# Kernel optimization log

Hardware: AMD Instinct MI355X
Metric: run time of the kernel (lower is better)

## Reference

```python
import jax, jax.numpy as jnp
import numpy as np

H = 51      # lstm_out, hard-coded in the module
L = 3       # num_lstms
IN = 2      # input_dim = f_in(1) + f_time(1)
B = 1024
T = 2048


def _softplus(x):
    # log(1+exp(x)) with the module's inf guard (softplus==inf -> x),
    # written in a grad-safe clipped form (identical in fp32 range).
    x_safe = jnp.minimum(x, 30.0)
    return jnp.where(x > 30.0, x, jnp.log1p(jnp.exp(x_safe)))


def setup_inputs() -> dict:
    key = jax.random.key(0)
    ks = jax.random.split(key, 2 + 4 * L + 2)
    inp = {}
    inp["input"] = jax.random.normal(ks[0], (B, T, 1), dtype=jnp.float32)
    inp["time_idx"] = jax.random.normal(ks[1], (B, T, 1), dtype=jnp.float32)
    k = 1.0 / np.sqrt(H)  # PyTorch LSTMCell/Linear default init scale
    idx = 2
    for l in range(L):
        d_in = IN if l == 0 else H
        inp[f"W_ih{l}"] = jax.random.uniform(ks[idx], (4 * H, d_in), jnp.float32, -k, k); idx += 1
        inp[f"W_hh{l}"] = jax.random.uniform(ks[idx], (4 * H, H), jnp.float32, -k, k); idx += 1
        inp[f"b_ih{l}"] = jax.random.uniform(ks[idx], (4 * H,), jnp.float32, -k, k); idx += 1
        inp[f"b_hh{l}"] = jax.random.uniform(ks[idx], (4 * H,), jnp.float32, -k, k); idx += 1
    inp["W_lin"] = jax.random.uniform(ks[idx], (2, H), jnp.float32, -k, k); idx += 1
    inp["b_lin"] = jax.random.uniform(ks[idx], (2,), jnp.float32, -k, k)
    inp["future"] = 0
    return inp


def _cell(x_t, h, c, W_ih, W_hh, b_ih, b_hh):
    # PyTorch LSTMCell: gates in order i, f, g, o
    gates = x_t @ W_ih.T + b_ih + h @ W_hh.T + b_hh  # (B, 4H)
    i, f, g, o = jnp.split(gates, 4, axis=-1)
    c_new = jax.nn.sigmoid(f) * c + jax.nn.sigmoid(i) * jnp.tanh(g)
    h_new = jax.nn.sigmoid(o) * jnp.tanh(c_new)
    return h_new, c_new


def reference(input, time_idx,
              W_ih0, W_hh0, b_ih0, b_hh0,
              W_ih1, W_hh1, b_ih1, b_hh1,
              W_ih2, W_hh2, b_ih2, b_hh2,
              W_lin, b_lin, future):
    params = [(W_ih0, W_hh0, b_ih0, b_hh0),
              (W_ih1, W_hh1, b_ih1, b_hh1),
              (W_ih2, W_hh2, b_ih2, b_hh2)]
    bsz = input.shape[0]
    # future == 0: time_idx covers exactly the conditioning context
    x = jnp.concatenate([input, time_idx], axis=2)  # (B, T, IN)
    xs = jnp.swapaxes(x, 0, 1)                       # (T, B, IN)
    h0 = jnp.zeros((L, bsz, H), dtype=input.dtype)
    c0 = jnp.zeros((L, bsz, H), dtype=input.dtype)

    def step(carry, x_t):
        hs, cs = carry
        inp_l = x_t
        nh, nc = [], []
        for l, (Wih, Whh, bih, bhh) in enumerate(params):
            h_new, c_new = _cell(inp_l, hs[l], cs[l], Wih, Whh, bih, bhh)
            nh.append(h_new); nc.append(c_new)
            inp_l = h_new
        out = inp_l @ W_lin.T + b_lin  # (B, 2) from linear1
        return (jnp.stack(nh), jnp.stack(nc)), out

    _, outs = jax.lax.scan(step, (h0, c0), xs)  # (T, B, 2)
    outs = jnp.swapaxes(outs, 0, 1)             # (B, T, 2)
    mean = outs[..., 0]
    std = _softplus(outs[..., 1])               # positivity constraint on col 1
    return jnp.stack([mean, std], axis=-1)
```

## Files before the change

### kernel.cpp

```cpp
#include <hip/hip_runtime.h>
#include <cstddef>
#include <cstdint>

#define Hd 51
#define Td 2048
#define NBb 4
#define NTH 768
#define NBLK 256

typedef _Float16 f16x8 __attribute__((ext_vector_type(8)));
typedef _Float16 f16x4 __attribute__((ext_vector_type(4)));
typedef float    f32x4 __attribute__((ext_vector_type(4)));

#define RB0   128
#define RB12  256
#define BASE0 0
#define BASE1 4096
#define BASE2 12288
#define PRE   20480
#define LDSB  32768

#define LOG2E  1.44269504f
#define LOG2E2 2.88539008f

__device__ __forceinline__ int vaddr(int base, int rowB, int db, int n, int off) {
    return base + db * (16 * rowB) + ((off >> 4) << 8) + (n << 4) + (off & 15);
}

__device__ __forceinline__ int pslot(int kg, int r, int n) {
    return (r << 4) | ((kg >> 1) << 3) | ((kg & 1) << 2) | (n ^ r);
}

__device__ __forceinline__ float fast_rcp(float x) { return __builtin_amdgcn_rcpf(x); }
__device__ __forceinline__ float exp2_fast(float x) {
#if __has_builtin(__builtin_amdgcn_exp2f)
    return __builtin_amdgcn_exp2f(x);
#else
    return exp2f(x);
#endif
}

__device__ __forceinline__ float sigm2(float ap)  { return fast_rcp(1.f + exp2_fast(-ap)); }
__device__ __forceinline__ float tanh2(float ap)  { return fmaf(2.f, fast_rcp(1.f + exp2_fast(-ap)), -1.f); }
__device__ __forceinline__ float tanh_c(float x) {
    float e = exp2_fast(-LOG2E2 * fabsf(x));
    float t = (1.f - e) * fast_rcp(1.f + e);
    return copysignf(t, x);
}

__global__ __launch_bounds__(NTH, 3)
void lstm3_mfma(const float* __restrict__ g_input, const float* __restrict__ g_time,
                const float* __restrict__ Wih0, const float* __restrict__ Whh0,
                const float* __restrict__ bih0, const float* __restrict__ bhh0,
                const float* __restrict__ Wih1, const float* __restrict__ Whh1,
                const float* __restrict__ bih1, const float* __restrict__ bhh1,
                const float* __restrict__ Wih2, const float* __restrict__ Whh2,
                const float* __restrict__ bih2, const float* __restrict__ bhh2,
                const float* __restrict__ Wlin, const float* __restrict__ blin,
                float* __restrict__ g_out)
{
    __shared__ __align__(16) unsigned char lds[LDSB];

    const int tid  = threadIdx.x;
    const int lane = tid & 63;
    const int w    = tid >> 6;
    const int g    = w >> 2;
    const int c    = w & 3;
    const int ncol = lane & 15;
    const int kg   = lane >> 4;
    const int b0   = blockIdx.x * NBb;

    for (int i = tid * 4; i < LDSB; i += NTH * 4) *(uint32_t*)(lds + i) = 0u;
    __syncthreads();

    if (tid < 32) {
        int db = tid >> 4, n = tid & 15;
        *(unsigned short*)(lds + vaddr(BASE0, RB0,  db, n,  54 * 2)) = 0x3C00;
        *(unsigned short*)(lds + vaddr(BASE1, RB12, db, n, 112 * 2)) = 0x3C00;
        *(unsigned short*)(lds + vaddr(BASE2, RB12, db, n, 112 * 2)) = 0x3C00;
    } else if (tid >= 64 && tid < 72) {
        int i = tid - 64; int n = i & 3, f = i >> 2;
        const float* src = f ? g_time : g_input;
        float v = src[(size_t)(b0 + n) * Td];
        *(_Float16*)(lds + vaddr(BASE0, RB0, 0, n, (52 + f) * 2)) = (_Float16)v;
    }

    const int er = 16 * c + ncol;
    const bool rvalid = (er < Hd);
    f16x8 AF[16];

    if (g == 0) {
        #pragma unroll
        for (int gs = 0; gs < 4; ++gs) {
            const int sr = gs * Hd + er;
            const float S = (gs == 2) ? LOG2E2 : LOG2E;
            #pragma unroll
            for (int s = 0; s < 2; ++s)
                #pragma unroll
                for (int e = 0; e < 8; ++e) {
                    const int kk = 32 * s + 8 * kg + e;
                    float v = 0.f;
                    if (rvalid) {
                        if (kk < 51)                   v = Whh0[sr * 51 + kk];
                        else if (kk == 52 || kk == 53) v = Wih0[sr * 2 + (kk - 52)];
                        else if (kk == 54)             v = bih0[sr] + bhh0[sr];
                    }
                    AF[gs * 2 + s][e] = (_Float16)(v * S);
                }
        }
    } else {
        const float* Wih = (g == 1) ? Wih1 : Wih2;
        const float* Whh = (g == 1) ? Whh1 : Whh2;
        const float* bihp = (g == 1) ? bih1 : bih2;
        const float* bhhp = (g == 1) ? bhh1 : bhh2;
        #pragma unroll
        for (int gs = 0; gs < 4; ++gs) {
            const int sr = gs * Hd + er;
            const float S = (gs == 2) ? LOG2E2 : LOG2E;
            #pragma unroll
            for (int s = 0; s < 4; ++s)
                #pragma unroll
                for (int e = 0; e < 8; ++e) {
                    const int kk = 32 * s + 8 * kg + e;
                    float v = 0.f;
                    float sc = S;
                    if (rvalid) {
                        if (kk < 51)                   v = Wih[sr * 51 + kk];
                        else if (kk >= 56 && kk < 107) v = Whh[sr * 51 + (kk - 56)];
                        else if (kk == 112)            v = bihp[sr] + bhhp[sr];
                    } else if (g == 2 && gs == 0 && (er == 52 || er == 53)) {
                        const int hr = er - 52;
                        sc = 1.f;
                        if (kk >= 56 && kk < 107)      v = Wlin[hr * 51 + (kk - 56)];
                        else if (kk == 112)            v = blin[hr];
                    }
                    AF[gs * 4 + s][e] = (_Float16)(v * sc);
                }
        }
    }

    const f32x4 Z = {0.f, 0.f, 0.f, 0.f};
    const int PAR0 = 16 * RB0;
    const int PAR12 = 16 * RB12;
    int rd0a = vaddr(BASE0, RB0, 0, ncol, 16 * kg);
    int rd0b = vaddr(BASE0, RB0, 0, ncol, 64 + 16 * kg);
    int rd12[4];
    {
        const int baseg = (g == 2) ? BASE2 : BASE1;
        #pragma unroll
        for (int s = 0; s < 4; ++s) rd12[s] = vaddr(baseg, RB12, 0, ncol, 64 * s + 16 * kg);
    }
    const int e0 = 16 * c + 4 * kg;
    int pw[4];
    bool pwok[4];
    #pragma unroll
    for (int r = 0; r < 4; ++r) {
        pw[r] = PRE + ((g * 4 + c) << 10) + (pslot(kg, r, ncol & 3) << 4);
        pwok[r] = (ncol < 4) && (e0 + r < Hd);
    }

    const bool uok = (lane < 51);
    int ul = 0, prd = 0, wh1 = 0, wh2 = 0, str1 = 0;
    bool has2 = false;
    if (uok) {
        const int u = lane * 12 + w;
        ul = u / 204;
        const int rr = u % 204;
        const int ue = rr >> 2;
        const int un = rr & 3;
        const int cc = ue >> 4, kk = (ue >> 2) & 3, r2 = ue & 3;
        prd = PRE + ((ul * 4 + cc) << 10) + (pslot(kk, r2, un) << 4);
        if (ul == 0) {
            wh1 = vaddr(BASE0, RB0,  0, un, 2 * ue);       str1 = PAR0;
            wh2 = vaddr(BASE1, RB12, 0, un, 2 * ue);       has2 = true;
        } else if (ul == 1) {
            wh1 = vaddr(BASE1, RB12, 0, un, 112 + 2 * ue); str1 = PAR12;
            wh2 = vaddr(BASE2, RB12, 0, un, 2 * ue);       has2 = true;
        } else {
            wh1 = vaddr(BASE2, RB12, 0, un, 112 + 2 * ue); str1 = PAR12;
        }
    }
    float ucs = 0.f;

    __syncthreads();

    for (int n = 0; n <= Td + 2; ++n) {
        const int rb = n & 1, wb = rb ^ 1;
        const int rP0 = rb * PAR0, rP12 = rb * PAR12;

        if (g == 0) {
            const bool dopf = (w == 0 && lane < 8 && (n + 1) < Td);
            float pfv = 0.f;
            const int nb = lane & 3, f = lane >> 2;
            if (dopf) {
                const float* src = f ? g_time : g_input;
                pfv = src[(size_t)(b0 + nb) * Td + (n + 1)];
            }
            if (n < Td) {
                f16x8 B0 = *(const f16x8*)(lds + rd0a + rP0);
                f16x8 B1 = *(const f16x8*)(lds + rd0b + rP0);
                f32x4 a_i = Z, a_f = Z, a_g = Z, a_o = Z;
                __builtin_amdgcn_s_setprio(1);
                a_i = __builtin_amdgcn_mfma_f32_16x16x32_f16(AF[0], B0, a_i, 0, 0, 0);
                a_i = __builtin_amdgcn_mfma_f32_16x16x32_f16(AF[1], B1, a_i, 0, 0, 0);
                a_f = __builtin_amdgcn_mfma_f32_16x16x32_f16(AF[2], B0, a_f, 0, 0, 0);
                a_f = __builtin_amdgcn_mfma_f32_16x16x32_f16(AF[3], B1, a_f, 0, 0, 0);
                a_g = __builtin_amdgcn_mfma_f32_16x16x32_f16(AF[4], B0, a_g, 0, 0, 0);
                a_g = __builtin_amdgcn_mfma_f32_16x16x32_f16(AF[5], B1, a_g, 0, 0, 0);
                a_o = __builtin_amdgcn_mfma_f32_16x16x32_f16(AF[6], B0, a_o, 0, 0, 0);
                a_o = __builtin_amdgcn_mfma_f32_16x16x32_f16(AF[7], B1, a_o, 0, 0, 0);
                __builtin_amdgcn_s_setprio(0);
                #pragma unroll
                for (int r = 0; r < 4; ++r)
                    if (pwok[r]) {
                        f32x4 v = {a_i[r], a_f[r], a_g[r], a_o[r]};
                        *(f32x4*)(lds + pw[r]) = v;
                    }
            }
            if (dopf)
                *(_Float16*)(lds + vaddr(BASE0, RB0, wb, nb, (52 + f) * 2)) = (_Float16)pfv;
        } else {
            const bool act = (g == 1) ? (n >= 1 && n <= Td) : (n >= 2);
            if (act) {
                f16x8 B[4];
                #pragma unroll
                for (int s = 0; s < 4; ++s)
                    B[s] = *(const f16x8*)(lds + rd12[s] + rP12);
                f32x4 a_i = Z, a_f = Z, a_g = Z, a_o = Z;
                __builtin_amdgcn_s_setprio(1);
                #pragma unroll
                for (int s = 0; s < 4; ++s) {
                    a_i = __builtin_amdgcn_mfma_f32_16x16x32_f16(AF[0 * 4 + s], B[s], a_i, 0, 0, 0);
                    a_f = __builtin_amdgcn_mfma_f32_16x16x32_f16(AF[1 * 4 + s], B[s], a_f, 0, 0, 0);
                    a_g = __builtin_amdgcn_mfma_f32_16x16x32_f16(AF[2 * 4 + s], B[s], a_g, 0, 0, 0);
                    a_o = __builtin_amdgcn_mfma_f32_16x16x32_f16(AF[3 * 4 + s], B[s], a_o, 0, 0, 0);
                }
                __builtin_amdgcn_s_setprio(0);
                #pragma unroll
                for (int r = 0; r < 4; ++r)
                    if (pwok[r]) {
                        f32x4 v = {a_i[r], a_f[r], a_g[r], a_o[r]};
                        *(f32x4*)(lds + pw[r]) = v;
                    }
                if (g == 2 && w == 11 && kg == 1 && ncol < 4 && n >= 3) {
                    float mean = a_i[0];
                    float spre = a_i[1];
                    float sp = (spre > 30.f) ? spre : __logf(1.f + __expf(spre));
                    const int t = n - 3;
                    float2 o2 = make_float2(mean, sp);
                    *(float2*)&g_out[((size_t)(b0 + ncol) * Td + t) * 2] = o2;
                }
            }
        }
        __syncthreads();

        if (uok) {
            const int t_u = n - ul;
            if (t_u >= 0 && t_u < Td) {
                f32x4 v = *(const f32x4*)(lds + prd);
                float si = sigm2(v[0]);
                float sf = sigm2(v[1]);
                float gg = tanh2(v[2]);
                float go = sigm2(v[3]);
                float cn = fmaf(sf, ucs, si * gg);
                ucs = cn;
                _Float16 hf = (_Float16)(go * tanh_c(cn));
                *(_Float16*)(lds + wh1 + wb * str1) = hf;
                if (has2) *(_Float16*)(lds + wh2 + wb * PAR12) = hf;
            }
        }
        __syncthreads();
    }
}

extern "C" void kernel_launch(void* const* d_in, const int* in_sizes, int n_in,
                              void* d_out, int out_size, void* d_ws, size_t ws_size,
                              hipStream_t stream) {
    const float* input = (const float*)d_in[0];
    const float* timei = (const float*)d_in[1];
    const float* Wih0  = (const float*)d_in[2];
    const float* Whh0  = (const float*)d_in[3];
    const float* bih0  = (const float*)d_in[4];
    const float* bhh0  = (const float*)d_in[5];
    const float* Wih1  = (const float*)d_in[6];
    const float* Whh1  = (const float*)d_in[7];
    const float* bih1  = (const float*)d_in[8];
    const float* bhh1  = (const float*)d_in[9];
    const float* Wih2  = (const float*)d_in[10];
    const float* Whh2  = (const float*)d_in[11];
    const float* bih2  = (const float*)d_in[12];
    const float* bhh2  = (const float*)d_in[13];
    const float* Wlin  = (const float*)d_in[14];
    const float* blin  = (const float*)d_in[15];
    float* out = (float*)d_out;

    lstm3_mfma<<<dim3(NBLK), dim3(NTH), 0, stream>>>(
        input, timei,
        Wih0, Whh0, bih0, bhh0,
        Wih1, Whh1, bih1, bhh1,
        Wih2, Whh2, bih2, bhh2,
        Wlin, blin, out);
}
```

Measured before the change: 2.028 ms.

## Remap LSTM update lanes to own layer and restrict B-fragment LDS loads

Reassigns the elementwise cell-update work so each warp updates units of its own layer (u = w*51+lane, layer = g) instead of striping units across all warps, and changes the gate-preactivation slot swizzle to match. B fragments are now loaded from LDS only by lanes with ncol<4 and kept in persistent registers (zero elsewhere), cutting redundant LDS reads since only four batch columns are real. The MFMA sequence for layers 1-2 is manually unrolled. This removes LDS bandwidth and cross-layer scatter, at the cost of extra registers and a new layout that must stay consistent.

```diff
diff --git a/kernel.cpp b/kernel.cpp
--- a/kernel.cpp
+++ b/kernel.cpp
@@ -27,8 +27,8 @@
     return base + db * (16 * rowB) + ((off >> 4) << 8) + (n << 4) + (off & 15);
 }
 
-__device__ __forceinline__ int pslot(int kg, int r, int n) {
-    return (r << 4) | ((kg >> 1) << 3) | ((kg & 1) << 2) | (n ^ r);
+__device__ __forceinline__ int pslot(int m4, int n) {
+    return ((m4 ^ n) & 15) | (n << 4);
 }
 
 __device__ __forceinline__ float fast_rcp(float x) { return __builtin_amdgcn_rcpf(x); }
@@ -155,25 +155,23 @@
     bool pwok[4];
     #pragma unroll
     for (int r = 0; r < 4; ++r) {
-        pw[r] = PRE + ((g * 4 + c) << 10) + (pslot(kg, r, ncol & 3) << 4);
+        pw[r] = PRE + ((g * 4 + c) << 10) + (pslot(4 * kg + r, ncol & 3) << 4);
         pwok[r] = (ncol < 4) && (e0 + r < Hd);
     }
 
     const bool uok = (lane < 51);
-    int ul = 0, prd = 0, wh1 = 0, wh2 = 0, str1 = 0;
+    int prd = 0, wh1 = 0, wh2 = 0, str1 = 0;
     bool has2 = false;
     if (uok) {
-        const int u = lane * 12 + w;
-        ul = u / 204;
-        const int rr = u % 204;
+        const int u  = w * 51 + lane;
+        const int rr = u - g * 204;
         const int ue = rr >> 2;
         const int un = rr & 3;
-        const int cc = ue >> 4, kk = (ue >> 2) & 3, r2 = ue & 3;
-        prd = PRE + ((ul * 4 + cc) << 10) + (pslot(kk, r2, un) << 4);
-        if (ul == 0) {
+        prd = PRE + ((g * 4 + (ue >> 4)) << 10) + (pslot(ue & 15, un) << 4);
+        if (g == 0) {
             wh1 = vaddr(BASE0, RB0,  0, un, 2 * ue);       str1 = PAR0;
             wh2 = vaddr(BASE1, RB12, 0, un, 2 * ue);       has2 = true;
-        } else if (ul == 1) {
+        } else if (g == 1) {
             wh1 = vaddr(BASE1, RB12, 0, un, 112 + 2 * ue); str1 = PAR12;
             wh2 = vaddr(BASE2, RB12, 0, un, 2 * ue);       has2 = true;
         } else {
@@ -181,6 +179,12 @@
         }
     }
     float ucs = 0.f;
+
+    f16x8 zf;
+    #pragma unroll
+    for (int e = 0; e < 8; ++e) zf[e] = (_Float16)0.f;
+    f16x8 B0 = zf, B1 = zf;
+    f16x8 Bv0 = zf, Bv1 = zf, Bv2 = zf, Bv3 = zf;
 
     __syncthreads();
 
@@ -197,8 +201,10 @@
                 pfv = src[(size_t)(b0 + nb) * Td + (n + 1)];
             }
             if (n < Td) {
-                f16x8 B0 = *(const f16x8*)(lds + rd0a + rP0);
-                f16x8 B1 = *(const f16x8*)(lds + rd0b + rP0);
+                if (ncol < 4) {
+                    B0 = *(const f16x8*)(lds + rd0a + rP0);
+                    B1 = *(const f16x8*)(lds + rd0b + rP0);
+                }
                 f32x4 a_i = Z, a_f = Z, a_g = Z, a_o = Z;
                 __builtin_amdgcn_s_setprio(1);
                 a_i = __builtin_amdgcn_mfma_f32_16x16x32_f16(AF[0], B0, a_i, 0, 0, 0);
@@ -222,19 +228,30 @@
         } else {
             const bool act = (g == 1) ? (n >= 1 && n <= Td) : (n >= 2);
             if (act) {
-                f16x8 B[4];
-                #pragma unroll
-                for (int s = 0; s < 4; ++s)
-                    B[s] = *(const f16x8*)(lds + rd12[s] + rP12);
+                if (ncol < 4) {
+                    Bv0 = *(const f16x8*)(lds + rd12[0] + rP12);
+                    Bv1 = *(const f16x8*)(lds + rd12[1] + rP12);
+                    Bv2 = *(const f16x8*)(lds + rd12[2] + rP12);
+                    Bv3 = *(const f16x8*)(lds + rd12[3] + rP12);
+                }
                 f32x4 a_i = Z, a_f = Z, a_g = Z, a_o = Z;
                 __builtin_amdgcn_s_setprio(1);
-                #pragma unroll
-                for (int s = 0; s < 4; ++s) {
-                    a_i = __builtin_amdgcn_mfma_f32_16x16x32_f16(AF[0 * 4 + s], B[s], a_i, 0, 0, 0);
-                    a_f = __builtin_amdgcn_mfma_f32_16x16x32_f16(AF[1 * 4 + s], B[s], a_f, 0, 0, 0);
-                    a_g = __builtin_amdgcn_mfma_f32_16x16x32_f16(AF[2 * 4 + s], B[s], a_g, 0, 0, 0);
-                    a_o = __builtin_amdgcn_mfma_f32_16x16x32_f16(AF[3 * 4 + s], B[s], a_o, 0, 0, 0);
-                }
+                a_i = __builtin_amdgcn_mfma_f32_16x16x32_f16(AF[0],  Bv0, a_i, 0, 0, 0);
+                a_f = __builtin_amdgcn_mfma_f32_16x16x32_f16(AF[4],  Bv0, a_f, 0, 0, 0);
+                a_g = __builtin_amdgcn_mfma_f32_16x16x32_f16(AF[8],  Bv0, a_g, 0, 0, 0);
+                a_o = __builtin_amdgcn_mfma_f32_16x16x32_f16(AF[12], Bv0, a_o, 0, 0, 0);
+                a_i = __builtin_amdgcn_mfma_f32_16x16x32_f16(AF[1],  Bv1, a_i, 0, 0, 0);
+                a_f = __builtin_amdgcn_mfma_f32_16x16x32_f16(AF[5],  Bv1, a_f, 0, 0, 0);
+                a_g = __builtin_amdgcn_mfma_f32_16x16x32_f16(AF[9],  Bv1, a_g, 0, 0, 0);
+                a_o = __builtin_amdgcn_mfma_f32_16x16x32_f16(AF[13], Bv1, a_o, 0, 0, 0);
+                a_i = __builtin_amdgcn_mfma_f32_16x16x32_f16(AF[2],  Bv2, a_i, 0, 0, 0);
+                a_f = __builtin_amdgcn_mfma_f32_16x16x32_f16(AF[6],  Bv2, a_f, 0, 0, 0);
+                a_g = __builtin_amdgcn_mfma_f32_16x16x32_f16(AF[10], Bv2, a_g, 0, 0, 0);
+                a_o = __builtin_amdgcn_mfma_f32_16x16x32_f16(AF[14], Bv2, a_o, 0, 0, 0);
+                a_i = __builtin_amdgcn_mfma_f32_16x16x32_f16(AF[3],  Bv3, a_i, 0, 0, 0);
+                a_f = __builtin_amdgcn_mfma_f32_16x16x32_f16(AF[7],  Bv3, a_f, 0, 0, 0);
+                a_g = __builtin_amdgcn_mfma_f32_16x16x32_f16(AF[11], Bv3, a_g, 0, 0, 0);
+                a_o = __builtin_amdgcn_mfma_f32_16x16x32_f16(AF[15], Bv3, a_o, 0, 0, 0);
                 __builtin_amdgcn_s_setprio(0);
                 #pragma unroll
                 for (int r = 0; r < 4; ++r)
@@ -255,7 +272,7 @@
         __syncthreads();
 
         if (uok) {
-            const int t_u = n - ul;
+            const int t_u = n - g;
             if (t_u >= 0 && t_u < Td) {
                 f32x4 v = *(const f32x4*)(lds + prd);
                 float si = sigm2(v[0]);
```

Result: no change. 2.053 ms (+1.3%).
